# Performance work log

Measured on AMD Instinct MI355X. Metric: run time of the kernel, lower is better.

Reference implementation:

```python
import jax, jax.numpy as jnp
import numpy as np

NUM_PTS = 4
N_OFF = 4


def inverse_sigmoid(x, eps=1e-5):
    x = jnp.clip(x, 0.0, 1.0)
    return jnp.log(jnp.clip(x, eps, None) / jnp.clip(1.0 - x, eps, None))


def uniform_flat_indices(T, H, W, n):
    # torch: linspace(hop/2, D-1-hop/2, n).round().long(), meshed over (t,h,w)
    def ax(D):
        hop = D / n
        return jnp.round(jnp.linspace(hop / 2.0, D - 1.0 - hop / 2.0, n)).astype(jnp.int32)
    ti, hi, wi = ax(T), ax(H), ax(W)
    return ((ti[:, None, None] * H + hi[None, :, None]) * W + wi[None, None, :]).reshape(-1)


def _normalized_thw(idx, T, H, W):
    wn = (idx % W).astype(jnp.float32) / (W - 1)
    hn = ((idx // W) % H).astype(jnp.float32) / (H - 1)
    tn = (idx // (W * H)).astype(jnp.float32) / (T - 1)
    return jnp.stack([tn, hn, wn], axis=-1)


def grid_sample_3d(inp, grid):
    # Matches torch F.grid_sample 5D, bilinear, padding zeros, align_corners=False.
    # inp: (N,C,D,H,W); grid: (N,Do,Ho,Wo,3) with grid[...,0]=x->W, 1=y->H, 2=z->D
    N, C, D, H, W = inp.shape
    Do, Ho, Wo = grid.shape[1:4]
    P = Do * Ho * Wo
    g = grid.reshape(N, P, 3)
    ix = ((g[..., 0] + 1.0) * W - 1.0) * 0.5
    iy = ((g[..., 1] + 1.0) * H - 1.0) * 0.5
    iz = ((g[..., 2] + 1.0) * D - 1.0) * 0.5
    x0 = jnp.floor(ix); y0 = jnp.floor(iy); z0 = jnp.floor(iz)
    fx = ix - x0; fy = iy - y0; fz = iz - z0
    x0i = x0.astype(jnp.int32); y0i = y0.astype(jnp.int32); z0i = z0.astype(jnp.int32)
    inp_flat = inp.reshape(N, C, D * H * W)
    out = jnp.zeros((N, C, P), inp.dtype)
    for dz in (0, 1):
        for dy in (0, 1):
            for dx in (0, 1):
                xi = x0i + dx; yi = y0i + dy; zi = z0i + dz
                w = (fx if dx else 1.0 - fx) * (fy if dy else 1.0 - fy) * (fz if dz else 1.0 - fz)
                valid = (xi >= 0) & (xi < W) & (yi >= 0) & (yi < H) & (zi >= 0) & (zi < D)
                flat = (jnp.clip(zi, 0, D - 1) * H + jnp.clip(yi, 0, H - 1)) * W + jnp.clip(xi, 0, W - 1)
                vals = jnp.take_along_axis(inp_flat, jnp.broadcast_to(flat[:, None, :], (N, C, P)), axis=2)
                out = out + vals * (w * valid.astype(inp.dtype))[:, None, :]
    return out.reshape(N, C, Do, Ho, Wo)


def forward(features, pos, W1, b1, W2, b2, Wn, bn, Wl, bl, Woff, boff, Ww, bw, gamma, beta):
    B, C, T, H, Wd, L = features.shape
    THW = T * H * Wd
    No = N_OFF
    N = NUM_PTS ** 3
    d = C // No
    BLNo = B * L * No

    flat = uniform_flat_indices(T, H, Wd, NUM_PTS)                    # (N,)
    ind_pts = jnp.broadcast_to(flat[None, None, :], (B, L, N))

    feats_l = jnp.transpose(features, (0, 5, 2, 3, 4, 1)).reshape(B, L, THW, C)
    pos_l = jnp.transpose(pos, (0, 5, 2, 3, 4, 1)).reshape(B, L, THW, C)
    sampled_pts = feats_l[:, :, flat, :]                              # (B,L,N,C)
    sampled_pos = pos_l[:, :, flat, :]
    glob = jnp.transpose(jnp.mean(features, axis=(2, 3, 4)), (0, 2, 1))  # (B,L,C)
    glob = jnp.broadcast_to(glob[:, :, None, :], (B, L, N, C))

    off_src = jnp.concatenate([sampled_pts, sampled_pos, glob], axis=-1)
    off_src = jax.nn.relu(off_src @ W1 + b1)
    off_src = jax.nn.relu(off_src @ W2 + b2)                          # (B,L,N,C)

    nxt = off_src @ Wn + bn                                           # (B,L,N,3)
    w_l = jax.nn.softmax(off_src @ Wl + bl, axis=-1)                  # (B,L,N,L)

    osr = off_src.reshape(B, L, N, No, d).transpose(0, 1, 3, 2, 4).reshape(BLNo, N, d)
    offset = osr @ Woff + boff                                        # (BLNo,N,3)
    w_o = jax.nn.softmax(osr @ Ww + bw, axis=-1)[..., 1:]             # (BLNo,N,1)

    # --- build flow field: identity grid with sampled coords scattered in ---
    idx = jnp.broadcast_to(ind_pts[:, :, None, :], (B, L, No, N)).reshape(BLNo, N)
    thw = _normalized_thw(idx, T, H, Wd)
    samp = jax.nn.sigmoid(inverse_sigmoid(thw) + offset) * 2.0 - 1.0  # (BLNo,N,3)
    mesh = jnp.stack(jnp.meshgrid(jnp.linspace(-1.0, 1.0, T), jnp.linspace(-1.0, 1.0, H), jnp.linspace(-1.0, 1.0, Wd), indexing='ij'), axis=-1).reshape(THW, 3)
    base = jnp.broadcast_to(mesh[None], (BLNo, THW, 3))
    bI = jnp.arange(BLNo)[:, None]
    flow = base.at[bI, idx].set(samp).reshape(BLNo, T, H, Wd, 3)

    feats_rep = jnp.transpose(features, (0, 5, 1, 2, 3, 4))           # (B,L,C,T,H,W)
    feats_rep = jnp.broadcast_to(feats_rep[:, :, None], (B, L, No, C, T, H, Wd)).reshape(BLNo, C, T, H, Wd)
    sf = grid_sample_3d(feats_rep, flow)                              # (BLNo,C,T,H,W)
    sf = jnp.transpose(sf, (0, 2, 3, 4, 1))                           # (BLNo,T,H,W,C)

    wo_full = jnp.zeros((BLNo, THW, 1), features.dtype).at[bI, idx].set(w_o).reshape(BLNo, T, H, Wd, 1)
    wsf = (sf * wo_full).reshape(B, L, No, T, H, Wd, C).sum(axis=2)   # (B,L,T,H,W,C)
    feats2 = features + jnp.transpose(wsf, (0, 5, 2, 3, 4, 1))        # (B,C,T,H,W,L)

    # level weights scattered then summed over target-level axis l
    bI2 = jnp.arange(B)[:, None, None]
    lI2 = jnp.arange(L)[None, :, None]
    wl_full = jnp.zeros((B, L, THW, L), features.dtype).at[bI2, lI2, ind_pts].set(w_l)
    wl_sum = wl_full.sum(axis=-1).reshape(B, L, T, H, Wd)             # (B,L,T,H,W)
    feats3 = feats2 * jnp.transpose(wl_sum, (0, 2, 3, 4, 1))[:, None] # broadcast over C

    # LayerNorm over channel dim (transpose(1,-1) in torch)
    x = jnp.transpose(feats3, (0, 5, 2, 3, 4, 1))                     # (B,L,T,H,W,C)
    mu = jnp.mean(x, axis=-1, keepdims=True)
    var = jnp.var(x, axis=-1, keepdims=True)
    xn = (x - mu) * jax.lax.rsqrt(var + 1e-5) * gamma + beta
    feats_out = jnp.transpose(xn, (0, 5, 2, 3, 4, 1))

    # offset_adder -> next flattened indices
    thw2 = _normalized_thw(ind_pts, T, H, Wd)
    disp = jax.nn.sigmoid(inverse_sigmoid(thw2) + nxt)
    scale = jnp.array([T - 1, H - 1, Wd - 1], jnp.float32)
    di = jnp.round(disp * scale).astype(jnp.int32)
    next_ind = H * Wd * di[..., 0] + Wd * di[..., 1] + di[..., 2]
    return feats_out, next_ind


def setup_inputs():
    key = jax.random.key(0)
    ks = jax.random.split(key, 10)
    B, C, T, H, W, L = 1, 256, 8, 32, 32, 4
    s = 0.02
    d = C // N_OFF
    return {
        'features': jax.random.normal(ks[0], (B, C, T, H, W, L), jnp.float32),
        'pos': jax.random.normal(ks[1], (B, C, T, H, W, L), jnp.float32),
        'W1': jax.random.normal(ks[2], (3 * C, C), jnp.float32) * s,
        'b1': jnp.zeros((C,), jnp.float32),
        'W2': jax.random.normal(ks[3], (C, C), jnp.float32) * s,
        'b2': jnp.zeros((C,), jnp.float32),
        'Wn': jax.random.normal(ks[4], (C, 3), jnp.float32) * s,
        'bn': jnp.zeros((3,), jnp.float32),
        'Wl': jax.random.normal(ks[5], (C, L), jnp.float32) * s,
        'bl': jnp.zeros((L,), jnp.float32),
        'Woff': jax.random.normal(ks[6], (d, 3), jnp.float32) * s,
        'boff': jnp.zeros((3,), jnp.float32),
        'Ww': jax.random.normal(ks[7], (d, 2), jnp.float32) * s,
        'bw': jnp.zeros((2,), jnp.float32),
        'gamma': jnp.ones((C,), jnp.float32),
        'beta': jnp.zeros((C,), jnp.float32),
    }


def reference(features, pos, W1, b1, W2, b2, Wn, bn, Wl, bl, Woff, boff, Ww, bw, gamma, beta):
    return forward(features, pos, W1, b1, W2, b2, Wn, bn, Wl, bl, Woff, boff, Ww, bw, gamma, beta)
```

## Files before the change

kernel.cpp:

```cpp
#include <hip/hip_runtime.h>
#include <math.h>

#define CDIM 256
#define TDIM 8
#define HDIM 32
#define WDIM 32
#define LDIM 4
#define THW 8192
#define CSTR 32768
#define NS 64
#define OUT0_SIZE 8388608

#define G1_KS 64
#define G1_KB 12
#define G2_KS 32
#define G2_KB 8

__device__ __constant__ int c_ti[4] = {1, 3, 4, 6};
__device__ __constant__ int c_hw[4] = {4, 12, 19, 27};

__device__ __forceinline__ float sigm(float x) { return 1.f / (1.f + expf(-x)); }

__device__ __forceinline__ float wave_sum64(float x) {
#pragma unroll
    for (int s = 32; s > 0; s >>= 1) x += __shfl_xor(x, s, 64);
    return x;
}

__global__ void k_fill_part(const float* __restrict__ feat, const float* __restrict__ beta,
                            float* __restrict__ out, float4* __restrict__ partF) {
    int c = blockIdx.x >> 3, part = blockIdx.x & 7;
    float bv = beta[c];
    float4 bf = make_float4(bv, bv, bv, bv);
    const float4* f = (const float4*)(feat + (size_t)c * CSTR) + part * 1024;
    float4* o = (float4*)(out + (size_t)c * CSTR) + part * 1024;
    float4 a = make_float4(0.f, 0.f, 0.f, 0.f);
#pragma unroll
    for (int it = 0; it < 4; ++it) {
        int i = it * 256 + threadIdx.x;
        float4 v = f[i];
        o[i] = bf;
        a.x += v.x; a.y += v.y; a.z += v.z; a.w += v.w;
    }
    __shared__ float4 sred[256];
    sred[threadIdx.x] = a;
    __syncthreads();
    for (int off = 128; off > 0; off >>= 1) {
        if (threadIdx.x < off) {
            float4 t = sred[threadIdx.x + off];
            sred[threadIdx.x].x += t.x; sred[threadIdx.x].y += t.y;
            sred[threadIdx.x].z += t.z; sred[threadIdx.x].w += t.w;
        }
        __syncthreads();
    }
    if (threadIdx.x == 0) partF[blockIdx.x] = sred[0];
}

__global__ void k_globred(const float4* __restrict__ partF, float* __restrict__ glob) {
    int l = blockIdx.x, c = threadIdx.x;
    float s = 0.f;
#pragma unroll
    for (int p = 0; p < 8; ++p) {
        float4 v = partF[c * 8 + p];
        s += (l == 0) ? v.x : (l == 1) ? v.y : (l == 2) ? v.z : v.w;
    }
    glob[l * CDIM + c] = s * (1.f / 8192.f);
}

__global__ void k_gemm1(const float* __restrict__ feat, const float* __restrict__ pos,
                        const float* __restrict__ glob, const float* __restrict__ W1,
                        float* __restrict__ p1) {
    __shared__ float sA[16][G1_KB];
    int mt = blockIdx.x >> 6, ks = blockIdx.x & 63;
    int k0 = ks * G1_KB;
    int t = threadIdx.x;
    if (t < 16 * G1_KB) {
        int i = t / G1_KB, kk = t - i * G1_KB;
        int k = k0 + kk;
        int m = mt * 16 + i, l = m >> 6, n = m & 63;
        int sp = (c_ti[n >> 4] * HDIM + c_hw[(n >> 2) & 3]) * WDIM + c_hw[n & 3];
        float val;
        if (k < 256)      val = feat[(size_t)k * CSTR + sp * LDIM + l];
        else if (k < 512) val = pos[(size_t)(k - 256) * CSTR + sp * LDIM + l];
        else              val = glob[l * CDIM + (k - 512)];
        sA[i][kk] = val;
    }
    __syncthreads();
    int j = t;
    float acc[16];
#pragma unroll
    for (int i = 0; i < 16; ++i) acc[i] = 0.f;
#pragma unroll
    for (int kk = 0; kk < G1_KB; ++kk) {
        float wv = W1[(size_t)(k0 + kk) * 256 + j];
#pragma unroll
        for (int i = 0; i < 16; ++i) acc[i] = fmaf(sA[i][kk], wv, acc[i]);
    }
#pragma unroll
    for (int i = 0; i < 16; ++i)
        p1[((size_t)(ks * 256 + mt * 16 + i)) * 256 + j] = acc[i];
}

__global__ void k_h1red(const float* __restrict__ p1, const float* __restrict__ b1,
                        float* __restrict__ h1) {
    int m = blockIdx.x, j = threadIdx.x;
    float v = b1[j];
#pragma unroll 8
    for (int s = 0; s < G1_KS; ++s) v += p1[((size_t)(s * 256 + m)) * 256 + j];
    h1[m * 256 + j] = fmaxf(v, 0.f);
}

__global__ void k_gemm2(const float* __restrict__ h1, const float* __restrict__ W2,
                        float* __restrict__ p2) {
    __shared__ float sH[8][G2_KB];
    int mt = blockIdx.x >> 5, ks = blockIdx.x & 31;
    int k0 = ks * G2_KB, m0 = mt * 8;
    int t = threadIdx.x;
    if (t < 64) {
        int i = t >> 3, kk = t & 7;
        sH[i][kk] = h1[(m0 + i) * 256 + k0 + kk];
    }
    __syncthreads();
    int j = t;
    float acc[8];
#pragma unroll
    for (int i = 0; i < 8; ++i) acc[i] = 0.f;
#pragma unroll
    for (int kk = 0; kk < G2_KB; ++kk) {
        float wv = W2[(size_t)(k0 + kk) * 256 + j];
#pragma unroll
        for (int i = 0; i < 8; ++i) acc[i] = fmaf(sH[i][kk], wv, acc[i]);
    }
#pragma unroll
    for (int i = 0; i < 8; ++i)
        p2[((size_t)(ks * 256 + m0 + i)) * 256 + j] = acc[i];
}

__global__ void k_heads_sample(const float* __restrict__ feat,
                               const float* __restrict__ p2, const float* __restrict__ b2,
                               const float* __restrict__ Wn, const float* __restrict__ bn,
                               const float* __restrict__ Woff, const float* __restrict__ boff,
                               const float* __restrict__ Ww, const float* __restrict__ bw,
                               const float* __restrict__ gamma, const float* __restrict__ beta,
                               float* __restrict__ out, float* __restrict__ next_out) {
    __shared__ float s_samp[4][3];
    __shared__ float s_wo[4];
    __shared__ float s_w[32];
    __shared__ int   s_o[32];
    __shared__ float red1[4], red2[4], redn[3][4];

    int m = blockIdx.x, l = m >> 6, n = m & 63;
    int j = threadIdx.x, o = j >> 6, r = j & 63;

    float v = b2[j];
#pragma unroll 8
    for (int s = 0; s < G2_KS; ++s) v += p2[((size_t)(s * 256 + m)) * 256 + j];
    v = fmaxf(v, 0.f);

    float pn0 = wave_sum64(v * Wn[j * 3 + 0]);
    float pn1 = wave_sum64(v * Wn[j * 3 + 1]);
    float pn2 = wave_sum64(v * Wn[j * 3 + 2]);
    if (r == 0) { redn[0][o] = pn0; redn[1][o] = pn1; redn[2][o] = pn2; }

    float po0 = wave_sum64(v * Woff[r * 3 + 0]);
    float po1 = wave_sum64(v * Woff[r * 3 + 1]);
    float po2 = wave_sum64(v * Woff[r * 3 + 2]);
    float z0  = wave_sum64(v * Ww[r * 2 + 0]);
    float z1  = wave_sum64(v * Ww[r * 2 + 1]);

    float tn = (float)c_ti[n >> 4] / 7.f;
    float hn = (float)c_hw[(n >> 2) & 3] / 31.f;
    float wn = (float)c_hw[n & 3] / 31.f;
    float lg0 = logf(tn / (1.f - tn));
    float lg1 = logf(hn / (1.f - hn));
    float lg2 = logf(wn / (1.f - wn));

    if (r == 0) {
        s_samp[o][0] = sigm(lg0 + po0 + boff[0]) * 2.f - 1.f;
        s_samp[o][1] = sigm(lg1 + po1 + boff[1]) * 2.f - 1.f;
        s_samp[o][2] = sigm(lg2 + po2 + boff[2]) * 2.f - 1.f;
        s_wo[o] = 1.f / (1.f + expf((z0 + bw[0]) - (z1 + bw[1])));
    }
    __syncthreads();

    if (j == 0) {
        float t0 = redn[0][0] + redn[0][1] + redn[0][2] + redn[0][3];
        float t1 = redn[1][0] + redn[1][1] + redn[1][2] + redn[1][3];
        float t2 = redn[2][0] + redn[2][1] + redn[2][2] + redn[2][3];
        float d0 = rintf(sigm(lg0 + t0 + bn[0]) * 7.f);
        float d1 = rintf(sigm(lg1 + t1 + bn[1]) * 31.f);
        float d2 = rintf(sigm(lg2 + t2 + bn[2]) * 31.f);
        next_out[m] = 1024.f * d0 + 32.f * d1 + d2;
    }

    if (j < 4) {
        int oo = j;
        float wv = s_wo[oo];
        float g0 = s_samp[oo][0], g1 = s_samp[oo][1], g2 = s_samp[oo][2];
        float ix = ((g0 + 1.f) * 32.f - 1.f) * 0.5f;
        float iy = ((g1 + 1.f) * 32.f - 1.f) * 0.5f;
        float iz = ((g2 + 1.f) * 8.f  - 1.f) * 0.5f;
        float x0f = floorf(ix), y0f = floorf(iy), z0f = floorf(iz);
        float fx = ix - x0f, fy = iy - y0f, fz = iz - z0f;
        int x0 = (int)x0f, y0 = (int)y0f, z0 = (int)z0f;
#pragma unroll
        for (int k = 0; k < 8; ++k) {
            int dx = k & 1, dy = (k >> 1) & 1, dz = k >> 2;
            int xi = x0 + dx, yi = y0 + dy, zi = z0 + dz;
            float w = (dx ? fx : 1.f - fx) * (dy ? fy : 1.f - fy) * (dz ? fz : 1.f - fz);
            bool valid = (xi >= 0) && (xi < WDIM) && (yi >= 0) && (yi < HDIM) && (zi >= 0) && (zi < TDIM);
            int xc = min(max(xi, 0), WDIM - 1);
            int yc = min(max(yi, 0), HDIM - 1);
            int zc = min(max(zi, 0), TDIM - 1);
            s_w[oo * 8 + k] = valid ? w * wv : 0.f;
            s_o[oo * 8 + k] = ((zc * HDIM + yc) * WDIM + xc) * LDIM + l;
        }
    }
    __syncthreads();

    int c = j;
    const float* fc = feat + (size_t)c * CSTR;
    int sp = (c_ti[n >> 4] * HDIM + c_hw[(n >> 2) & 3]) * WDIM + c_hw[n & 3];
    float acc = fc[sp * LDIM + l];
#pragma unroll
    for (int k = 0; k < 32; ++k) acc += s_w[k] * fc[s_o[k]];

    float s1 = acc, s2 = acc * acc;
#pragma unroll
    for (int d = 32; d > 0; d >>= 1) { s1 += __shfl_xor(s1, d, 64); s2 += __shfl_xor(s2, d, 64); }
    int wid = j >> 6;
    if ((j & 63) == 0) { red1[wid] = s1; red2[wid] = s2; }
    __syncthreads();
    float tot  = red1[0] + red1[1] + red1[2] + red1[3];
    float totq = red2[0] + red2[1] + red2[2] + red2[3];
    float mu = tot * (1.f / 256.f);
    float var = fmaxf(totq * (1.f / 256.f) - mu * mu, 0.f);
    float y = (acc - mu) * rsqrtf(var + 1e-5f) * gamma[c] + beta[c];
    out[(size_t)c * CSTR + sp * LDIM + l] = y;
}

extern "C" void kernel_launch(void* const* d_in, const int* in_sizes, int n_in,
                              void* d_out, int out_size, void* d_ws, size_t ws_size,
                              hipStream_t stream) {
    const float* feat = (const float*)d_in[0];
    const float* pos  = (const float*)d_in[1];
    const float* W1   = (const float*)d_in[2];
    const float* b1   = (const float*)d_in[3];
    const float* W2   = (const float*)d_in[4];
    const float* b2   = (const float*)d_in[5];
    const float* Wn   = (const float*)d_in[6];
    const float* bn   = (const float*)d_in[7];
    const float* Woff = (const float*)d_in[10];
    const float* boff = (const float*)d_in[11];
    const float* Ww   = (const float*)d_in[12];
    const float* bw   = (const float*)d_in[13];
    const float* gamma= (const float*)d_in[14];
    const float* beta = (const float*)d_in[15];
    float* out = (float*)d_out;
    float* next_out = out + OUT0_SIZE;

    float* ws    = (float*)d_ws;
    float4* partF= (float4*)ws;
    float* glob  = ws + 8192;
    float* h1    = glob + 1024;
    float* p1    = h1 + 65536;
    float* p2    = p1 + (size_t)G1_KS * 65536;

    k_fill_part<<<2048, 256, 0, stream>>>(feat, beta, out, partF);
    k_globred<<<4, 256, 0, stream>>>(partF, glob);
    k_gemm1<<<16 * G1_KS, 256, 0, stream>>>(feat, pos, glob, W1, p1);
    k_h1red<<<256, 256, 0, stream>>>(p1, b1, h1);
    k_gemm2<<<32 * G2_KS, 256, 0, stream>>>(h1, W2, p2);
    k_heads_sample<<<256, 256, 0, stream>>>(feat, p2, b2, Wn, bn, Woff, boff, Ww, bw,
                                            gamma, beta, out, next_out);
}
```

Measured before the change: 159.5 us.

## Replace split-K GEMMs with in-block K reduction and transposed gathered input

```diff
diff --git a/kernel.cpp b/kernel.cpp
--- a/kernel.cpp
+++ b/kernel.cpp
@@ -11,11 +11,6 @@
 #define NS 64
 #define OUT0_SIZE 8388608
 
-#define G1_KS 64
-#define G1_KB 12
-#define G2_KS 32
-#define G2_KB 8
-
 __device__ __constant__ int c_ti[4] = {1, 3, 4, 6};
 __device__ __constant__ int c_hw[4] = {4, 12, 19, 27};
 
@@ -27,8 +22,9 @@
     return x;
 }
 
-__global__ void k_fill_part(const float* __restrict__ feat, const float* __restrict__ beta,
-                            float* __restrict__ out, float4* __restrict__ partF) {
+__global__ void __launch_bounds__(256)
+k_fill_part(const float* __restrict__ feat, const float* __restrict__ beta,
+            float* __restrict__ out, float4* __restrict__ partF) {
     int c = blockIdx.x >> 3, part = blockIdx.x & 7;
     float bv = beta[c];
     float4 bf = make_float4(bv, bv, bv, bv);
@@ -42,107 +38,96 @@
         o[i] = bf;
         a.x += v.x; a.y += v.y; a.z += v.z; a.w += v.w;
     }
-    __shared__ float4 sred[256];
-    sred[threadIdx.x] = a;
-    __syncthreads();
-    for (int off = 128; off > 0; off >>= 1) {
-        if (threadIdx.x < off) {
-            float4 t = sred[threadIdx.x + off];
-            sred[threadIdx.x].x += t.x; sred[threadIdx.x].y += t.y;
-            sred[threadIdx.x].z += t.z; sred[threadIdx.x].w += t.w;
+#pragma unroll
+    for (int s = 32; s > 0; s >>= 1) {
+        a.x += __shfl_xor(a.x, s, 64);
+        a.y += __shfl_xor(a.y, s, 64);
+        a.z += __shfl_xor(a.z, s, 64);
+        a.w += __shfl_xor(a.w, s, 64);
+    }
+    __shared__ float4 sw[4];
+    if ((threadIdx.x & 63) == 0) sw[threadIdx.x >> 6] = a;
+    __syncthreads();
+    if (threadIdx.x == 0) {
+        float4 r;
+        r.x = sw[0].x + sw[1].x + sw[2].x + sw[3].x;
+        r.y = sw[0].y + sw[1].y + sw[2].y + sw[3].y;
+        r.z = sw[0].z + sw[1].z + sw[2].z + sw[3].z;
+        r.w = sw[0].w + sw[1].w + sw[2].w + sw[3].w;
+        partF[blockIdx.x] = r;
+    }
+}
+
+__global__ void __launch_bounds__(256)
+k_gather(const float* __restrict__ feat, const float* __restrict__ pos,
+         const float4* __restrict__ partF, float* __restrict__ in1T) {
+    int m = blockIdx.x, l = m >> 6, n = m & 63;
+    int sp = (c_ti[n >> 4] * HDIM + c_hw[(n >> 2) & 3]) * WDIM + c_hw[n & 3];
+    int t = threadIdx.x;
+    in1T[(size_t)t * 256 + m] = feat[(size_t)t * CSTR + sp * LDIM + l];
+    in1T[(size_t)(256 + t) * 256 + m] = pos[(size_t)t * CSTR + sp * LDIM + l];
+    float s = 0.f;
+#pragma unroll
+    for (int p = 0; p < 8; ++p) {
+        float4 v = partF[t * 8 + p];
+        s += (l == 0) ? v.x : (l == 1) ? v.y : (l == 2) ? v.z : v.w;
+    }
+    in1T[(size_t)(512 + t) * 256 + m] = s * (1.f / 8192.f);
+}
+
+template <int KITER, int WRITE_T>
+__global__ void __launch_bounds__(256)
+k_gemm(const float* __restrict__ AT, const float* __restrict__ Wt,
+       const float* __restrict__ bias, float* __restrict__ outp) {
+    __shared__ float sAcc[256][33];
+    int mt = blockIdx.x >> 4, jt = blockIdx.x & 15;
+    int m0 = mt * 16, j0 = jt * 16;
+    int t = threadIdx.x;
+    int j8 = t & 7, kq = t >> 3;
+    int j = j0 + j8 * 2;
+    float acc0[16], acc1[16];
+#pragma unroll
+    for (int i = 0; i < 16; ++i) { acc0[i] = 0.f; acc1[i] = 0.f; }
+#pragma unroll 4
+    for (int kk = 0; kk < KITER; ++kk) {
+        int k = kq + (kk << 5);
+        const float4* ap = (const float4*)(AT + (size_t)k * 256 + m0);
+        float av[16];
+        ((float4*)av)[0] = ap[0];
+        ((float4*)av)[1] = ap[1];
+        ((float4*)av)[2] = ap[2];
+        ((float4*)av)[3] = ap[3];
+        float2 w = *(const float2*)(Wt + (size_t)k * 256 + j);
+#pragma unroll
+        for (int i = 0; i < 16; ++i) {
+            acc0[i] = fmaf(av[i], w.x, acc0[i]);
+            acc1[i] = fmaf(av[i], w.y, acc1[i]);
         }
-        __syncthreads();
-    }
-    if (threadIdx.x == 0) partF[blockIdx.x] = sred[0];
-}
-
-__global__ void k_globred(const float4* __restrict__ partF, float* __restrict__ glob) {
-    int l = blockIdx.x, c = threadIdx.x;
-    float s = 0.f;
-#pragma unroll
-    for (int p = 0; p < 8; ++p) {
-        float4 v = partF[c * 8 + p];
-        s += (l == 0) ? v.x : (l == 1) ? v.y : (l == 2) ? v.z : v.w;
-    }
-    glob[l * CDIM + c] = s * (1.f / 8192.f);
-}
-
-__global__ void k_gemm1(const float* __restrict__ feat, const float* __restrict__ pos,
-                        const float* __restrict__ glob, const float* __restrict__ W1,
-                        float* __restrict__ p1) {
-    __shared__ float sA[16][G1_KB];
-    int mt = blockIdx.x >> 6, ks = blockIdx.x & 63;
-    int k0 = ks * G1_KB;
-    int t = threadIdx.x;
-    if (t < 16 * G1_KB) {
-        int i = t / G1_KB, kk = t - i * G1_KB;
-        int k = k0 + kk;
-        int m = mt * 16 + i, l = m >> 6, n = m & 63;
-        int sp = (c_ti[n >> 4] * HDIM + c_hw[(n >> 2) & 3]) * WDIM + c_hw[n & 3];
-        float val;
-        if (k < 256)      val = feat[(size_t)k * CSTR + sp * LDIM + l];
-        else if (k < 512) val = pos[(size_t)(k - 256) * CSTR + sp * LDIM + l];
-        else              val = glob[l * CDIM + (k - 512)];
-        sA[i][kk] = val;
-    }
-    __syncthreads();
-    int j = t;
-    float acc[16];
-#pragma unroll
-    for (int i = 0; i < 16; ++i) acc[i] = 0.f;
-#pragma unroll
-    for (int kk = 0; kk < G1_KB; ++kk) {
-        float wv = W1[(size_t)(k0 + kk) * 256 + j];
-#pragma unroll
-        for (int i = 0; i < 16; ++i) acc[i] = fmaf(sA[i][kk], wv, acc[i]);
-    }
-#pragma unroll
-    for (int i = 0; i < 16; ++i)
-        p1[((size_t)(ks * 256 + mt * 16 + i)) * 256 + j] = acc[i];
-}
-
-__global__ void k_h1red(const float* __restrict__ p1, const float* __restrict__ b1,
-                        float* __restrict__ h1) {
-    int m = blockIdx.x, j = threadIdx.x;
-    float v = b1[j];
-#pragma unroll 8
-    for (int s = 0; s < G1_KS; ++s) v += p1[((size_t)(s * 256 + m)) * 256 + j];
-    h1[m * 256 + j] = fmaxf(v, 0.f);
-}
-
-__global__ void k_gemm2(const float* __restrict__ h1, const float* __restrict__ W2,
-                        float* __restrict__ p2) {
-    __shared__ float sH[8][G2_KB];
-    int mt = blockIdx.x >> 5, ks = blockIdx.x & 31;
-    int k0 = ks * G2_KB, m0 = mt * 8;
-    int t = threadIdx.x;
-    if (t < 64) {
-        int i = t >> 3, kk = t & 7;
-        sH[i][kk] = h1[(m0 + i) * 256 + k0 + kk];
-    }
-    __syncthreads();
-    int j = t;
-    float acc[8];
-#pragma unroll
-    for (int i = 0; i < 8; ++i) acc[i] = 0.f;
-#pragma unroll
-    for (int kk = 0; kk < G2_KB; ++kk) {
-        float wv = W2[(size_t)(k0 + kk) * 256 + j];
-#pragma unroll
-        for (int i = 0; i < 8; ++i) acc[i] = fmaf(sH[i][kk], wv, acc[i]);
-    }
-#pragma unroll
-    for (int i = 0; i < 8; ++i)
-        p2[((size_t)(ks * 256 + m0 + i)) * 256 + j] = acc[i];
-}
-
-__global__ void k_heads_sample(const float* __restrict__ feat,
-                               const float* __restrict__ p2, const float* __restrict__ b2,
-                               const float* __restrict__ Wn, const float* __restrict__ bn,
-                               const float* __restrict__ Woff, const float* __restrict__ boff,
-                               const float* __restrict__ Ww, const float* __restrict__ bw,
-                               const float* __restrict__ gamma, const float* __restrict__ beta,
-                               float* __restrict__ out, float* __restrict__ next_out) {
+    }
+#pragma unroll
+    for (int i = 0; i < 16; ++i) {
+        sAcc[i * 16 + j8 * 2 + 0][kq] = acc0[i];
+        sAcc[i * 16 + j8 * 2 + 1][kq] = acc1[i];
+    }
+    __syncthreads();
+    int i = t >> 4, jj = t & 15;
+    float v = bias[j0 + jj];
+#pragma unroll
+    for (int q = 0; q < 32; ++q) v += sAcc[t][q];
+    v = fmaxf(v, 0.f);
+    if (WRITE_T)
+        outp[(size_t)(j0 + jj) * 256 + m0 + i] = v;
+    else
+        outp[(size_t)(m0 + i) * 256 + j0 + jj] = v;
+}
+
+__global__ void __launch_bounds__(256)
+k_heads_sample(const float* __restrict__ feat, const float* __restrict__ osrc,
+               const float* __restrict__ Wn, const float* __restrict__ bn,
+               const float* __restrict__ Woff, const float* __restrict__ boff,
+               const float* __restrict__ Ww, const float* __restrict__ bw,
+               const float* __restrict__ gamma, const float* __restrict__ beta,
+               float* __restrict__ out, float* __restrict__ next_out) {
     __shared__ float s_samp[4][3];
     __shared__ float s_wo[4];
     __shared__ float s_w[32];
@@ -152,10 +137,7 @@
     int m = blockIdx.x, l = m >> 6, n = m & 63;
     int j = threadIdx.x, o = j >> 6, r = j & 63;
 
-    float v = b2[j];
-#pragma unroll 8
-    for (int s = 0; s < G2_KS; ++s) v += p2[((size_t)(s * 256 + m)) * 256 + j];
-    v = fmaxf(v, 0.f);
+    float v = osrc[(size_t)m * 256 + j];
 
     float pn0 = wave_sum64(v * Wn[j * 3 + 0]);
     float pn1 = wave_sum64(v * Wn[j * 3 + 1]);
@@ -261,16 +243,14 @@
 
     float* ws    = (float*)d_ws;
     float4* partF= (float4*)ws;
-    float* glob  = ws + 8192;
-    float* h1    = glob + 1024;
-    float* p1    = h1 + 65536;
-    float* p2    = p1 + (size_t)G1_KS * 65536;
+    float* in1T  = ws + 8192;
+    float* h1T   = in1T + 196608;
+    float* osrc  = h1T + 65536;
 
     k_fill_part<<<2048, 256, 0, stream>>>(feat, beta, out, partF);
-    k_globred<<<4, 256, 0, stream>>>(partF, glob);
-    k_gemm1<<<16 * G1_KS, 256, 0, stream>>>(feat, pos, glob, W1, p1);
-    k_h1red<<<256, 256, 0, stream>>>(p1, b1, h1);
-    k_gemm2<<<32 * G2_KS, 256, 0, stream>>>(h1, W2, p2);
-    k_heads_sample<<<256, 256, 0, stream>>>(feat, p2, b2, Wn, bn, Woff, boff, Ww, bw,
+    k_gather<<<256, 256, 0, stream>>>(feat, pos, partF, in1T);
+    k_gemm<24, 1><<<256, 256, 0, stream>>>(in1T, W1, b1, h1T);
+    k_gemm<8, 0><<<256, 256, 0, stream>>>(h1T, W2, b2, osrc);
+    k_heads_sample<<<256, 256, 0, stream>>>(feat, osrc, Wn, bn, Woff, boff, Ww, bw,
                                             gamma, beta, out, next_out);
 }
```

Measured after the change: 154.9 us. -2.9%, faster.
